# Kernel optimization log

Measured on AMD Instinct MI355X. Metric: run time of the kernel, lower is better.

Reference implementation:

```python
import jax, jax.numpy as jnp
import numpy as np

N = 50000      # nodes
E = 800000     # edges (avg degree 16)
IN, HID, OUT = 256, 128, 64
K, ALPHA = 4, 0.0  # APPNPConv(k=4, alpha=0.0)


def setup_inputs() -> dict:
    key = jax.random.key(0)
    ks = jax.random.split(key, 5)
    features = jax.random.normal(ks[0], (N, IN), jnp.float32)
    src = jax.random.randint(ks[1], (E,), 0, N, jnp.int32)
    dst = jax.random.randint(ks[2], (E,), 0, N, jnp.int32)
    W1 = jax.random.normal(ks[3], (IN, HID), jnp.float32) / np.float32(np.sqrt(IN))
    b1 = jnp.zeros((HID,), jnp.float32)
    W3 = jax.random.normal(ks[4], (HID, OUT), jnp.float32) / np.float32(np.sqrt(HID))
    b3 = jnp.zeros((OUT,), jnp.float32)
    return dict(features=features, src=src, dst=dst, W1=W1, b1=b1, W3=W3, b3=b3)


def _sym_norms(src, dst, n):
    # D_out^{-1/2} for source side, D_in^{-1/2} for destination side (DGL norm='both')
    ones = jnp.ones((src.shape[0],), jnp.float32)
    deg_out = jax.ops.segment_sum(ones, src, num_segments=n)
    deg_in = jax.ops.segment_sum(ones, dst, num_segments=n)
    return jnp.clip(deg_out, 1.0) ** -0.5, jnp.clip(deg_in, 1.0) ** -0.5


def _prop(x, src, dst, norm_src, norm_dst):
    # x: [N, D]. Symmetric-normalized SpMM: D_in^{-1/2} A D_out^{-1/2} x
    msg = (x * norm_src[:, None])[src]                       # [E, D] gather
    agg = jax.ops.segment_sum(msg, dst, num_segments=x.shape[0])  # [N, D] scatter-add
    return agg * norm_dst[:, None]


def reference(features, src, dst, W1, b1, W3, b3):
    ns, nd = _sym_norms(src, dst, N)
    # GraphConv 1 (weight-first since in_dim > hidden_dim; math identical either way)
    h = _prop(features @ W1, src, dst, ns, nd) + b1
    # dropout is identity in eval mode (training=False)
    # APPNPConv: k=4 power-iteration steps with teleport alpha=0.0
    h0 = h
    for _ in range(K):
        h = (1.0 - ALPHA) * _prop(h, src, dst, ns, nd) + ALPHA * h0
    # GraphConv 3
    out = _prop(h @ W3, src, dst, ns, nd) + b3
    return out
```

## Files before the change

### kernel.cpp

```cpp
#include <hip/hip_runtime.h>
#include <math.h>

#define N_NODES 50000
#define N_EDGES 800000
#define DIN 256
#define DHID 128
#define DOUT 64
#define CSTRIDE 64
#define ZROW N_NODES
#define HBLOCKS 256
#define HCHUNK (N_EDGES / HBLOCKS)
#define HWORDS (N_NODES / 4)
#define SLICE ((size_t)(N_NODES + 1) * 16)
#define NGROUPS (N_NODES / 4)
#define P2BLOCKS 196

#define SB_SENT 3125
#define SB_HS (SB_SENT + HBLOCKS)
#define SB_HD (SB_HS + HBLOCKS)
#define SB_TOT (SB_HD + 66)

__global__ void k_setup(const int* __restrict__ src, const int* __restrict__ dst,
                        unsigned int* __restrict__ pS, unsigned int* __restrict__ pD,
                        unsigned int* __restrict__ csr32,
                        const float* __restrict__ W1, const float* __restrict__ b1,
                        const float* __restrict__ W3,
                        float* __restrict__ W13, float* __restrict__ bb,
                        float* __restrict__ Y0, float* __restrict__ Y1) {
    __shared__ unsigned int h[HWORDS];
    int bx = blockIdx.x, t = threadIdx.x;
    if (bx < SB_SENT) {
        unsigned int v = (unsigned int)ZROW | ((unsigned int)ZROW << 16);
        uint2 o; o.x = v; o.y = v;
        ((uint2*)csr32)[bx * 256 + t] = o;
        return;
    }
    if (bx < SB_HD) {
        const int* idx = (bx < SB_HS) ? src : dst;
        unsigned int* outp = (bx < SB_HS) ? pS : pD;
        int hb = bx - ((bx < SB_HS) ? SB_SENT : SB_HS);
        for (int w = t; w < HWORDS; w += 256) h[w] = 0u;
        __syncthreads();
        int base = hb * HCHUNK;
        for (int i = t; i < HCHUNK; i += 256) {
            int s = idx[base + i];
            atomicAdd(&h[s >> 2], 1u << ((s & 3) << 3));
        }
        __syncthreads();
        outp += (size_t)hb * HWORDS;
        for (int w = t; w < HWORDS; w += 256) outp[w] = h[w];
        return;
    }
    int vb = bx - SB_HD;
    if (vb == 65) {
        if (t < 64) {
            int qq = t >> 4, c2 = t & 15;
            Y0[(size_t)qq * SLICE + ((size_t)ZROW << 4) + c2] = 0.f;
            Y1[(size_t)qq * SLICE + ((size_t)ZROW << 4) + c2] = 0.f;
        }
        return;
    }
    if (vb == 64) {
        if (t < DOUT) {
            float s = 0.f;
            for (int k = 0; k < DHID; ++k) s += b1[k] * W3[k * DOUT + t];
            bb[t] = s;
        }
        return;
    }
    int idx2 = vb * 256 + t;
    int i = idx2 >> 6, j = idx2 & 63;
    float s = 0.f;
    for (int k = 0; k < DHID; ++k) s += W1[i * DHID + k] * W3[k * DOUT + j];
    W13[idx2] = s;
}

__global__ void k_hpre(const unsigned int* __restrict__ pS,
                       const unsigned int* __restrict__ pD,
                       unsigned int* __restrict__ prefix,
                       int* __restrict__ deg_in,
                       float* __restrict__ ns, float* __restrict__ nd,
                       float* __restrict__ cc, int* __restrict__ dparts) {
    __shared__ unsigned int sdw[64][4];
    __shared__ unsigned int sow[64][4];
    __shared__ int lh[65];
    int t = threadIdx.x;
    if (t < 65) lh[t] = 0;
    int col = t >> 2, sub = t & 3;
    int wid = blockIdx.x * 64 + col;
    bool act = wid < HWORDS;
    unsigned int ps = 0, pd = 0;
    if (act) {
        int b0 = sub << 6;
#pragma unroll 4
        for (int b = b0; b < b0 + 64; ++b) {
            ps += pS[(size_t)b * HWORDS + wid];
            pd += pD[(size_t)b * HWORDS + wid];
        }
    }
    sdw[col][sub] = pd;
    sow[col][sub] = ps;
    __syncthreads();
    if (act) {
        unsigned int base = 0;
        for (int k = 0; k < sub; ++k) base += sdw[col][k];
        int b0 = sub << 6;
        unsigned int run = base;
        for (int b = b0; b < b0 + 64; ++b) {
            unsigned int w = pD[(size_t)b * HWORDS + wid];
            prefix[(size_t)b * HWORDS + wid] = run;
            run += w;
        }
        if (sub == 0) {
            unsigned int totd = sdw[col][0] + sdw[col][1] + sdw[col][2] + sdw[col][3];
            unsigned int toto = sow[col][0] + sow[col][1] + sow[col][2] + sow[col][3];
            unsigned int di[4] = {totd & 0xffu, (totd >> 8) & 0xffu,
                                  (totd >> 16) & 0xffu, totd >> 24};
            unsigned int dov[4] = {toto & 0xffu, (toto >> 8) & 0xffu,
                                   (toto >> 16) & 0xffu, toto >> 24};
            int4 dd; dd.x = (int)di[0]; dd.y = (int)di[1]; dd.z = (int)di[2]; dd.w = (int)di[3];
            *(int4*)(deg_in + (wid << 2)) = dd;
            float4 vns, vnd, vcc;
            float* pns = &vns.x; float* pnd = &vnd.x; float* pcc = &vcc.x;
#pragma unroll
            for (int q = 0; q < 4; ++q) {
                int bin = (int)di[q]; if (bin > 64) bin = 64;
                atomicAdd(&lh[bin], 1);
                unsigned int a = dov[q] < 1u ? 1u : dov[q];
                unsigned int b = di[q] < 1u ? 1u : di[q];
                float fa = 1.0f / sqrtf((float)a);
                float fb = 1.0f / sqrtf((float)b);
                pns[q] = fa; pnd[q] = fb; pcc[q] = fa * fb;
            }
            *(float4*)(ns + (wid << 2)) = vns;
            *(float4*)(nd + (wid << 2)) = vnd;
            *(float4*)(cc + (wid << 2)) = vcc;
        }
    }
    __syncthreads();
    if (t < 65) dparts[blockIdx.x * 65 + t] = lh[t];
}

__global__ void k_dscan(const int* __restrict__ dparts, int* __restrict__ offs) {
    __shared__ int colsum[65], binbase[65];
    int t = threadIdx.x;
    if (t < 65) {
        int s = 0;
        for (int b = 0; b < P2BLOCKS; ++b) s += dparts[b * 65 + t];
        colsum[t] = s;
    }
    __syncthreads();
    if (t == 0) {
        int run = 0;
        for (int k = 64; k >= 0; --k) { binbase[k] = run; run += colsum[k]; }
    }
    __syncthreads();
    if (t < 65) {
        int run = binbase[t];
        for (int b = 0; b < P2BLOCKS; ++b) { offs[b * 65 + t] = run; run += dparts[b * 65 + t]; }
    }
}

__global__ void k_dscatter(const int* __restrict__ deg_in, const int* __restrict__ offs,
                           const float* __restrict__ cc, const float* __restrict__ ns,
                           const float* __restrict__ nd,
                           int* __restrict__ perm, int* __restrict__ inv,
                           int* __restrict__ degP, float* __restrict__ ccP,
                           float* __restrict__ nsP, float* __restrict__ ndP) {
    __shared__ int off[65];
    int t = threadIdx.x;
    if (t < 65) off[t] = offs[blockIdx.x * 65 + t];
    __syncthreads();
    int wid = blockIdx.x * 64 + t;
    if (t < 64 && wid < HWORDS) {
        int4 d4 = *(const int4*)(deg_in + (wid << 2));
        int dd[4] = {d4.x, d4.y, d4.z, d4.w};
#pragma unroll
        for (int k = 0; k < 4; ++k) {
            int node = (wid << 2) + k;
            int bin = dd[k] > 64 ? 64 : dd[k];
            int slot = atomicAdd(&off[bin], 1);
            perm[slot] = node; inv[node] = slot;
            degP[slot] = dd[k];
            ccP[slot] = cc[node]; nsP[slot] = ns[node]; ndP[slot] = nd[node];
        }
    }
}

__global__ void k_fill(const int* __restrict__ src, const int* __restrict__ dst,
                       const unsigned int* __restrict__ prefix,
                       const int* __restrict__ inv,
                       unsigned short* __restrict__ csr) {
    __shared__ unsigned int h[HWORDS];
    int t = threadIdx.x;
    const unsigned int* prow = prefix + (size_t)blockIdx.x * HWORDS;
    for (int w = t; w < HWORDS; w += 256) h[w] = prow[w];
    __syncthreads();
    int base = blockIdx.x * HCHUNK;
    for (int i = t; i < HCHUNK; i += 256) {
        int s = src[base + i], d = dst[base + i];
        int sh = (d & 3) << 3;
        unsigned int old = atomicAdd(&h[d >> 2], 1u << sh);
        int slot = (int)((old >> sh) & 0xffu);
        csr[((size_t)inv[d] << 6) + slot] = (unsigned short)inv[s];
    }
}

__global__ void k_gemm(const float* __restrict__ X, const float* __restrict__ W13,
                       const float* __restrict__ ns, const int* __restrict__ inv,
                       float* __restrict__ Y) {
    __shared__ float As[16][68];
    __shared__ float Bs[16][64];
    int tid = threadIdx.x;
    int tx = tid & 15, ty = tid >> 4;
    int row0 = blockIdx.x * 64;
    float acc[4][4];
#pragma unroll
    for (int i = 0; i < 4; ++i)
#pragma unroll
        for (int j = 0; j < 4; ++j) acc[i][j] = 0.f;

    int lr = tid >> 2;
    int lk = (tid & 3) << 2;
    int arow = row0 + lr;
    if (arow > N_NODES - 1) arow = N_NODES - 1;

    for (int k0 = 0; k0 < DIN; k0 += 16) {
        float4 a = *(const float4*)(X + (size_t)arow * DIN + k0 + lk);
        As[lk + 0][lr] = a.x; As[lk + 1][lr] = a.y;
        As[lk + 2][lr] = a.z; As[lk + 3][lr] = a.w;
        float4 b = *(const float4*)(W13 + (size_t)(k0 + (tid >> 4)) * DOUT + ((tid & 15) << 2));
        *(float4*)&Bs[tid >> 4][(tid & 15) << 2] = b;
        __syncthreads();
#pragma unroll
        for (int k = 0; k < 16; ++k) {
            float4 av = *(const float4*)&As[k][ty << 2];
            float4 bv = *(const float4*)&Bs[k][tx << 2];
            float ar[4] = {av.x, av.y, av.z, av.w};
            float br[4] = {bv.x, bv.y, bv.z, bv.w};
#pragma unroll
            for (int i = 0; i < 4; ++i)
#pragma unroll
                for (int j = 0; j < 4; ++j) acc[i][j] += ar[i] * br[j];
        }
        __syncthreads();
    }
    int qq = tx >> 2;
    int co = (tx & 3) << 2;
#pragma unroll
    for (int i = 0; i < 4; ++i) {
        int row = row0 + (ty << 2) + i;
        if (row < N_NODES) {
            float nsr = ns[row];
            int prow = inv[row];
            float4 o;
            o.x = acc[i][0] * nsr; o.y = acc[i][1] * nsr;
            o.z = acc[i][2] * nsr; o.w = acc[i][3] * nsr;
            *(float4*)(Y + (size_t)qq * SLICE + ((size_t)prow << 4) + co) = o;
        }
    }
}


template <int MODE>
__launch_bounds__(256, 8)
__global__ void k_spmm(const float* __restrict__ xs, float* __restrict__ ys,
                       const unsigned short* __restrict__ csr,
                       const int* __restrict__ degP,
                       const float* __restrict__ ccP, const float* __restrict__ nsP,
                       const float* __restrict__ ndP,
                       const float* __restrict__ bb, const float* __restrict__ b3,
                       const int* __restrict__ perm) {
    __shared__ unsigned short rows[4][256];
    int wid  = threadIdx.x >> 6;
    int lane = threadIdx.x & 63;
    int q    = (blockIdx.x & 7) >> 1;
    int half = blockIdx.x & 1;
    int g    = (blockIdx.x >> 3) * 8 + wid * 2 + half;
    if (g >= NGROUPS) return;
    int node0 = g << 2;

    int nn = lane >> 4, sl = lane & 15;
    const uint2* crow = (const uint2*)(csr + ((size_t)(node0 + nn) << 6)) + sl;
    uint2 rv = *crow;
    unsigned short* bp = &rows[wid][(sl << 4) + nn];
    bp[0]  = (unsigned short)(rv.x & 0xffffu);
    bp[4]  = (unsigned short)(rv.x >> 16);
    bp[8]  = (unsigned short)(rv.y & 0xffffu);
    bp[12] = (unsigned short)(rv.y >> 16);

    int n0u = __builtin_amdgcn_readfirstlane(node0);
    int m = (degP[n0u] + 7) & ~7;

    int n = lane >> 4, e = (lane >> 2) & 3, c4 = lane & 3;
    const unsigned short* rd = &rows[wid][(e << 2) + n];
    const float* xq = xs + (size_t)q * SLICE + (c4 << 2);

    float ax = 0.f, ay = 0.f, az = 0.f, aw = 0.f;
#define LDV(T) const float4 v##T = *(const float4*)(xq + ((size_t)rd[16 * (T)] << 4))
#define ACCV(T) ax += v##T.x; ay += v##T.y; az += v##T.z; aw += v##T.w
    if (m <= 8) {
        LDV(0); LDV(1);
        ACCV(0); ACCV(1);
    } else if (m <= 16) {
        LDV(0); LDV(1); LDV(2); LDV(3);
        ACCV(0); ACCV(1); ACCV(2); ACCV(3);
    } else if (m <= 24) {
        LDV(0); LDV(1); LDV(2); LDV(3); LDV(4); LDV(5);
        ACCV(0); ACCV(1); ACCV(2); ACCV(3); ACCV(4); ACCV(5);
    } else if (m <= 32) {
        LDV(0); LDV(1); LDV(2); LDV(3); LDV(4); LDV(5); LDV(6); LDV(7);
        ACCV(0); ACCV(1); ACCV(2); ACCV(3); ACCV(4); ACCV(5); ACCV(6); ACCV(7);
    } else {
        for (int j2 = 0; j2 < m; j2 += 8) {
            int o = j2 << 2;
            const float4 a = *(const float4*)(xq + ((size_t)rd[o] << 4));
            const float4 b = *(const float4*)(xq + ((size_t)rd[o + 16] << 4));
            ax += a.x; ay += a.y; az += a.z; aw += a.w;
            ax += b.x; ay += b.y; az += b.z; aw += b.w;
        }
    }
#undef LDV
#undef ACCV
    ax += __shfl_xor(ax, 4);  ay += __shfl_xor(ay, 4);
    az += __shfl_xor(az, 4);  aw += __shfl_xor(aw, 4);
    ax += __shfl_xor(ax, 8);  ay += __shfl_xor(ay, 8);
    az += __shfl_xor(az, 8);  aw += __shfl_xor(aw, 8);

    int nodeL = node0 + n;
    int colq  = (q << 4) + (c4 << 2);
    float4 r;
    if (MODE == 0) {
        float cv = ccP[nodeL], nv = nsP[nodeL];
        float4 bv = *(const float4*)(bb + colq);
        r.x = cv * ax + nv * bv.x; r.y = cv * ay + nv * bv.y;
        r.z = cv * az + nv * bv.z; r.w = cv * aw + nv * bv.w;
    } else if (MODE == 1) {
        float cv = ccP[nodeL];
        r.x = cv * ax; r.y = cv * ay; r.z = cv * az; r.w = cv * aw;
    } else {
        float dv = ndP[nodeL];
        float4 bv = *(const float4*)(b3 + colq);
        r.x = dv * ax + bv.x; r.y = dv * ay + bv.y;
        r.z = dv * az + bv.z; r.w = dv * aw + bv.w;
    }
    if (e == 0) {
        if (MODE == 2) {
            int orow = perm[nodeL];
            *(float4*)(ys + ((size_t)orow << 6) + colq) = r;
        } else {
            *(float4*)(ys + (size_t)q * SLICE + ((size_t)nodeL << 4) + (c4 << 2)) = r;
        }
    }
}


extern "C" void kernel_launch(void* const* d_in, const int* in_sizes, int n_in,
                              void* d_out, int out_size, void* d_ws, size_t ws_size,
                              hipStream_t stream) {
    const float* X   = (const float*)d_in[0];
    const int*   src = (const int*)d_in[1];
    const int*   dst = (const int*)d_in[2];
    const float* W1  = (const float*)d_in[3];
    const float* b1  = (const float*)d_in[4];
    const float* W3  = (const float*)d_in[5];
    const float* b3  = (const float*)d_in[6];
    float* out = (float*)d_out;

    char* ws = (char*)d_ws;
    size_t off = 0;
    auto alloc = [&](size_t bytes) -> void* {
        void* p = ws + off;
        off = (off + bytes + 255) & ~(size_t)255;
        return p;
    };
    unsigned int*   pS     = (unsigned int*)alloc((size_t)HBLOCKS * HWORDS * 4);
    unsigned int*   pD     = (unsigned int*)alloc((size_t)HBLOCKS * HWORDS * 4);
    unsigned int*   pref   = (unsigned int*)alloc((size_t)HBLOCKS * HWORDS * 4);
    float*          Y0     = (float*)alloc(SLICE * 4 * 4);
    float*          Y1     = (float*)alloc(SLICE * 4 * 4);
    unsigned short* csr    = (unsigned short*)alloc((size_t)N_NODES * CSTRIDE * 2);
    int*            deg_in = (int*)alloc((size_t)N_NODES * 4);
    float*          ns     = (float*)alloc((size_t)N_NODES * 4);
    float*          nd     = (float*)alloc((size_t)N_NODES * 4);
    float*          cc     = (float*)alloc((size_t)N_NODES * 4);
    int*            perm   = (int*)alloc((size_t)N_NODES * 4);
    int*            inv    = (int*)alloc((size_t)N_NODES * 4);
    int*            degP   = (int*)alloc((size_t)N_NODES * 4);
    float*          ccP    = (float*)alloc((size_t)N_NODES * 4);
    float*          nsP    = (float*)alloc((size_t)N_NODES * 4);
    float*          ndP    = (float*)alloc((size_t)N_NODES * 4);
    int*            dparts = (int*)alloc((size_t)P2BLOCKS * 65 * 4);
    int*            offs   = (int*)alloc((size_t)P2BLOCKS * 65 * 4);
    float*          W13    = (float*)alloc((size_t)DIN * DOUT * 4);
    float*          bb     = (float*)alloc(DOUT * 4);

    const int sblk = 1563 * 8;

    k_setup<<<SB_TOT, 256, 0, stream>>>(src, dst, pS, pD, (unsigned int*)csr,
                                        W1, b1, W3, W13, bb, Y0, Y1);
    k_hpre<<<P2BLOCKS, 256, 0, stream>>>(pS, pD, pref, deg_in, ns, nd, cc, dparts);
    k_dscan<<<1, 128, 0, stream>>>(dparts, offs);
    k_dscatter<<<P2BLOCKS, 128, 0, stream>>>(deg_in, offs, cc, ns, nd,
                                             perm, inv, degP, ccP, nsP, ndP);
    k_fill<<<HBLOCKS, 256, 0, stream>>>(src, dst, pref, inv, csr);

    k_gemm<<<(N_NODES + 63) / 64, 256, 0, stream>>>(X, W13, ns, inv, Y0);

    k_spmm<0><<<sblk, 256, 0, stream>>>(Y0, Y1, csr, degP, ccP, nsP, ndP, bb, b3, perm);
    k_spmm<1><<<sblk, 256, 0, stream>>>(Y1, Y0, csr, degP, ccP, nsP, ndP, bb, b3, perm);
    k_spmm<1><<<sblk, 256, 0, stream>>>(Y0, Y1, csr, degP, ccP, nsP, ndP, bb, b3, perm);
    k_spmm<1><<<sblk, 256, 0, stream>>>(Y1, Y0, csr, degP, ccP, nsP, ndP, bb, b3, perm);
    k_spmm<1><<<sblk, 256, 0, stream>>>(Y0, Y1, csr, degP, ccP, nsP, ndP, bb, b3, perm);
    k_spmm<2><<<sblk, 256, 0, stream>>>(Y1, out, csr, degP, ccP, nsP, ndP, bb, b3, perm);
}
```

Measured before the change: 304.3 us.

## Process two node groups per wavefront in SpMM, fold degree scan into scatter

Each SpMM wavefront now handles two groups of four degree-sorted nodes (eight nodes), loading both CSR row tiles and interleaving their gathers so more memory loads are in flight per wave. The grid size is halved to match. The separate single-block degree-scan kernel is removed, and each scatter block recomputes the column totals and its own prefix from the partial histograms, which saves a launch but repeats that work in every block. The histogram block count is halved, which changes the prefix-sum loop bounds. The risks are extra register pressure, and a load imbalance from sizing the unrolled path by the first node's degree when the second group can have a different degree.

```diff
diff --git a/kernel.cpp b/kernel.cpp
--- a/kernel.cpp
+++ b/kernel.cpp
@@ -8,11 +8,12 @@
 #define DOUT 64
 #define CSTRIDE 64
 #define ZROW N_NODES
-#define HBLOCKS 256
+#define HBLOCKS 128
 #define HCHUNK (N_EDGES / HBLOCKS)
 #define HWORDS (N_NODES / 4)
 #define SLICE ((size_t)(N_NODES + 1) * 16)
 #define NGROUPS (N_NODES / 4)
+#define NPAIRS (NGROUPS / 2)
 #define P2BLOCKS 196
 
 #define SB_SENT 3125
@@ -91,9 +92,9 @@
     bool act = wid < HWORDS;
     unsigned int ps = 0, pd = 0;
     if (act) {
-        int b0 = sub << 6;
+        int b0 = sub << 5;
 #pragma unroll 4
-        for (int b = b0; b < b0 + 64; ++b) {
+        for (int b = b0; b < b0 + 32; ++b) {
             ps += pS[(size_t)b * HWORDS + wid];
             pd += pD[(size_t)b * HWORDS + wid];
         }
@@ -104,9 +105,9 @@
     if (act) {
         unsigned int base = 0;
         for (int k = 0; k < sub; ++k) base += sdw[col][k];
-        int b0 = sub << 6;
+        int b0 = sub << 5;
         unsigned int run = base;
-        for (int b = b0; b < b0 + 64; ++b) {
+        for (int b = b0; b < b0 + 32; ++b) {
             unsigned int w = pD[(size_t)b * HWORDS + wid];
             prefix[(size_t)b * HWORDS + wid] = run;
             run += w;
@@ -141,35 +142,31 @@
     if (t < 65) dparts[blockIdx.x * 65 + t] = lh[t];
 }
 
-__global__ void k_dscan(const int* __restrict__ dparts, int* __restrict__ offs) {
-    __shared__ int colsum[65], binbase[65];
-    int t = threadIdx.x;
-    if (t < 65) {
-        int s = 0;
-        for (int b = 0; b < P2BLOCKS; ++b) s += dparts[b * 65 + t];
-        colsum[t] = s;
-    }
-    __syncthreads();
-    if (t == 0) {
-        int run = 0;
-        for (int k = 64; k >= 0; --k) { binbase[k] = run; run += colsum[k]; }
-    }
-    __syncthreads();
-    if (t < 65) {
-        int run = binbase[t];
-        for (int b = 0; b < P2BLOCKS; ++b) { offs[b * 65 + t] = run; run += dparts[b * 65 + t]; }
-    }
-}
-
-__global__ void k_dscatter(const int* __restrict__ deg_in, const int* __restrict__ offs,
+__global__ void k_dscatter(const int* __restrict__ deg_in, const int* __restrict__ dparts,
                            const float* __restrict__ cc, const float* __restrict__ ns,
                            const float* __restrict__ nd,
                            int* __restrict__ perm, int* __restrict__ inv,
                            int* __restrict__ degP, float* __restrict__ ccP,
                            float* __restrict__ nsP, float* __restrict__ ndP) {
-    __shared__ int off[65];
+    __shared__ int colsum[65], pre[65], off[65];
     int t = threadIdx.x;
-    if (t < 65) off[t] = offs[blockIdx.x * 65 + t];
+    if (t < 65) {
+        int tot = 0, pr = 0;
+        int mybx = (int)blockIdx.x;
+        for (int b = 0; b < P2BLOCKS; ++b) {
+            int v = dparts[b * 65 + t];
+            tot += v;
+            if (b < mybx) pr += v;
+        }
+        colsum[t] = tot; pre[t] = pr;
+    }
+    __syncthreads();
+    if (t == 0) {
+        int run = 0;
+        for (int k = 64; k >= 0; --k) { int c = colsum[k]; colsum[k] = run; run += c; }
+    }
+    __syncthreads();
+    if (t < 65) off[t] = colsum[t] + pre[t];
     __syncthreads();
     int wid = blockIdx.x * 64 + t;
     if (t < 64 && wid < HWORDS) {
@@ -271,85 +268,124 @@
                        const float* __restrict__ ndP,
                        const float* __restrict__ bb, const float* __restrict__ b3,
                        const int* __restrict__ perm) {
-    __shared__ unsigned short rows[4][256];
+    __shared__ unsigned short rows[4][512];
     int wid  = threadIdx.x >> 6;
     int lane = threadIdx.x & 63;
     int q    = (blockIdx.x & 7) >> 1;
     int half = blockIdx.x & 1;
-    int g    = (blockIdx.x >> 3) * 8 + wid * 2 + half;
-    if (g >= NGROUPS) return;
-    int node0 = g << 2;
+    int p    = (blockIdx.x >> 3) * 8 + wid * 2 + half;
+    if (p >= NPAIRS) return;
+    int node0 = p << 3;
 
     int nn = lane >> 4, sl = lane & 15;
-    const uint2* crow = (const uint2*)(csr + ((size_t)(node0 + nn) << 6)) + sl;
-    uint2 rv = *crow;
-    unsigned short* bp = &rows[wid][(sl << 4) + nn];
-    bp[0]  = (unsigned short)(rv.x & 0xffffu);
-    bp[4]  = (unsigned short)(rv.x >> 16);
-    bp[8]  = (unsigned short)(rv.y & 0xffffu);
-    bp[12] = (unsigned short)(rv.y >> 16);
+    const uint2* crowA = (const uint2*)(csr + ((size_t)(node0 + nn) << 6)) + sl;
+    const uint2* crowB = (const uint2*)(csr + ((size_t)(node0 + 4 + nn) << 6)) + sl;
+    uint2 rva = *crowA;
+    uint2 rvb = *crowB;
+    unsigned short* bpA = &rows[wid][(sl << 4) + nn];
+    unsigned short* bpB = bpA + 256;
+    bpA[0]  = (unsigned short)(rva.x & 0xffffu);
+    bpA[4]  = (unsigned short)(rva.x >> 16);
+    bpA[8]  = (unsigned short)(rva.y & 0xffffu);
+    bpA[12] = (unsigned short)(rva.y >> 16);
+    bpB[0]  = (unsigned short)(rvb.x & 0xffffu);
+    bpB[4]  = (unsigned short)(rvb.x >> 16);
+    bpB[8]  = (unsigned short)(rvb.y & 0xffffu);
+    bpB[12] = (unsigned short)(rvb.y >> 16);
 
     int n0u = __builtin_amdgcn_readfirstlane(node0);
     int m = (degP[n0u] + 7) & ~7;
 
     int n = lane >> 4, e = (lane >> 2) & 3, c4 = lane & 3;
-    const unsigned short* rd = &rows[wid][(e << 2) + n];
+    const unsigned short* rdA = &rows[wid][(e << 2) + n];
+    const unsigned short* rdB = rdA + 256;
     const float* xq = xs + (size_t)q * SLICE + (c4 << 2);
 
-    float ax = 0.f, ay = 0.f, az = 0.f, aw = 0.f;
-#define LDV(T) const float4 v##T = *(const float4*)(xq + ((size_t)rd[16 * (T)] << 4))
-#define ACCV(T) ax += v##T.x; ay += v##T.y; az += v##T.z; aw += v##T.w
+    float aAx = 0.f, aAy = 0.f, aAz = 0.f, aAw = 0.f;
+    float aBx = 0.f, aBy = 0.f, aBz = 0.f, aBw = 0.f;
+#define LDA(T) const float4 vA##T = *(const float4*)(xq + ((size_t)rdA[16 * (T)] << 4))
+#define LDB(T) const float4 vB##T = *(const float4*)(xq + ((size_t)rdB[16 * (T)] << 4))
+#define ACA(T) aAx += vA##T.x; aAy += vA##T.y; aAz += vA##T.z; aAw += vA##T.w
+#define ACB(T) aBx += vB##T.x; aBy += vB##T.y; aBz += vB##T.z; aBw += vB##T.w
     if (m <= 8) {
-        LDV(0); LDV(1);
-        ACCV(0); ACCV(1);
+        LDA(0); LDA(1); LDB(0); LDB(1);
+        ACA(0); ACA(1); ACB(0); ACB(1);
     } else if (m <= 16) {
-        LDV(0); LDV(1); LDV(2); LDV(3);
-        ACCV(0); ACCV(1); ACCV(2); ACCV(3);
+        LDA(0); LDA(1); LDA(2); LDA(3); LDB(0); LDB(1); LDB(2); LDB(3);
+        ACA(0); ACA(1); ACA(2); ACA(3); ACB(0); ACB(1); ACB(2); ACB(3);
     } else if (m <= 24) {
-        LDV(0); LDV(1); LDV(2); LDV(3); LDV(4); LDV(5);
-        ACCV(0); ACCV(1); ACCV(2); ACCV(3); ACCV(4); ACCV(5);
+        LDA(0); LDA(1); LDA(2); LDA(3); LDA(4); LDA(5);
+        LDB(0); LDB(1);
+        ACA(0); ACA(1); ACA(2); ACA(3);
+        LDB(2); LDB(3); LDB(4); LDB(5);
+        ACA(4); ACA(5);
+        ACB(0); ACB(1); ACB(2); ACB(3); ACB(4); ACB(5);
     } else if (m <= 32) {
-        LDV(0); LDV(1); LDV(2); LDV(3); LDV(4); LDV(5); LDV(6); LDV(7);
-        ACCV(0); ACCV(1); ACCV(2); ACCV(3); ACCV(4); ACCV(5); ACCV(6); ACCV(7);
+        LDA(0); LDA(1); LDA(2); LDA(3); LDB(0); LDB(1); LDB(2); LDB(3);
+        ACA(0); ACA(1); ACA(2); ACA(3); ACB(0); ACB(1); ACB(2); ACB(3);
+        LDA(4); LDA(5); LDA(6); LDA(7); LDB(4); LDB(5); LDB(6); LDB(7);
+        ACA(4); ACA(5); ACA(6); ACA(7); ACB(4); ACB(5); ACB(6); ACB(7);
     } else {
         for (int j2 = 0; j2 < m; j2 += 8) {
             int o = j2 << 2;
-            const float4 a = *(const float4*)(xq + ((size_t)rd[o] << 4));
-            const float4 b = *(const float4*)(xq + ((size_t)rd[o + 16] << 4));
-            ax += a.x; ay += a.y; az += a.z; aw += a.w;
-            ax += b.x; ay += b.y; az += b.z; aw += b.w;
-        }
-    }
-#undef LDV
-#undef ACCV
-    ax += __shfl_xor(ax, 4);  ay += __shfl_xor(ay, 4);
-    az += __shfl_xor(az, 4);  aw += __shfl_xor(aw, 4);
-    ax += __shfl_xor(ax, 8);  ay += __shfl_xor(ay, 8);
-    az += __shfl_xor(az, 8);  aw += __shfl_xor(aw, 8);
-
-    int nodeL = node0 + n;
+            const float4 a0 = *(const float4*)(xq + ((size_t)rdA[o] << 4));
+            const float4 a1 = *(const float4*)(xq + ((size_t)rdA[o + 16] << 4));
+            const float4 b0 = *(const float4*)(xq + ((size_t)rdB[o] << 4));
+            const float4 b1 = *(const float4*)(xq + ((size_t)rdB[o + 16] << 4));
+            aAx += a0.x; aAy += a0.y; aAz += a0.z; aAw += a0.w;
+            aAx += a1.x; aAy += a1.y; aAz += a1.z; aAw += a1.w;
+            aBx += b0.x; aBy += b0.y; aBz += b0.z; aBw += b0.w;
+            aBx += b1.x; aBy += b1.y; aBz += b1.z; aBw += b1.w;
+        }
+    }
+#undef LDA
+#undef LDB
+#undef ACA
+#undef ACB
+    aAx += __shfl_xor(aAx, 4);  aAy += __shfl_xor(aAy, 4);
+    aAz += __shfl_xor(aAz, 4);  aAw += __shfl_xor(aAw, 4);
+    aBx += __shfl_xor(aBx, 4);  aBy += __shfl_xor(aBy, 4);
+    aBz += __shfl_xor(aBz, 4);  aBw += __shfl_xor(aBw, 4);
+    aAx += __shfl_xor(aAx, 8);  aAy += __shfl_xor(aAy, 8);
+    aAz += __shfl_xor(aAz, 8);  aAw += __shfl_xor(aAw, 8);
+    aBx += __shfl_xor(aBx, 8);  aBy += __shfl_xor(aBy, 8);
+    aBz += __shfl_xor(aBz, 8);  aBw += __shfl_xor(aBw, 8);
+
+    int nodeA = node0 + n;
+    int nodeB = node0 + 4 + n;
     int colq  = (q << 4) + (c4 << 2);
-    float4 r;
+    float4 rA, rB;
     if (MODE == 0) {
-        float cv = ccP[nodeL], nv = nsP[nodeL];
         float4 bv = *(const float4*)(bb + colq);
-        r.x = cv * ax + nv * bv.x; r.y = cv * ay + nv * bv.y;
-        r.z = cv * az + nv * bv.z; r.w = cv * aw + nv * bv.w;
+        float cvA = ccP[nodeA], nvA = nsP[nodeA];
+        rA.x = cvA * aAx + nvA * bv.x; rA.y = cvA * aAy + nvA * bv.y;
+        rA.z = cvA * aAz + nvA * bv.z; rA.w = cvA * aAw + nvA * bv.w;
+        float cvB = ccP[nodeB], nvB = nsP[nodeB];
+        rB.x = cvB * aBx + nvB * bv.x; rB.y = cvB * aBy + nvB * bv.y;
+        rB.z = cvB * aBz + nvB * bv.z; rB.w = cvB * aBw + nvB * bv.w;
     } else if (MODE == 1) {
-        float cv = ccP[nodeL];
-        r.x = cv * ax; r.y = cv * ay; r.z = cv * az; r.w = cv * aw;
+        float cvA = ccP[nodeA];
+        rA.x = cvA * aAx; rA.y = cvA * aAy; rA.z = cvA * aAz; rA.w = cvA * aAw;
+        float cvB = ccP[nodeB];
+        rB.x = cvB * aBx; rB.y = cvB * aBy; rB.z = cvB * aBz; rB.w = cvB * aBw;
     } else {
-        float dv = ndP[nodeL];
         float4 bv = *(const float4*)(b3 + colq);
-        r.x = dv * ax + bv.x; r.y = dv * ay + bv.y;
-        r.z = dv * az + bv.z; r.w = dv * aw + bv.w;
+        float dvA = ndP[nodeA];
+        rA.x = dvA * aAx + bv.x; rA.y = dvA * aAy + bv.y;
+        rA.z = dvA * aAz + bv.z; rA.w = dvA * aAw + bv.w;
+        float dvB = ndP[nodeB];
+        rB.x = dvB * aBx + bv.x; rB.y = dvB * aBy + bv.y;
+        rB.z = dvB * aBz + bv.z; rB.w = dvB * aBw + bv.w;
     }
     if (e == 0) {
         if (MODE == 2) {
-            int orow = perm[nodeL];
-            *(float4*)(ys + ((size_t)orow << 6) + colq) = r;
+            int orowA = perm[nodeA];
+            int orowB = perm[nodeB];
+            *(float4*)(ys + ((size_t)orowA << 6) + colq) = rA;
+            *(float4*)(ys + ((size_t)orowB << 6) + colq) = rB;
         } else {
-            *(float4*)(ys + (size_t)q * SLICE + ((size_t)nodeL << 4) + (c4 << 2)) = r;
+            *(float4*)(ys + (size_t)q * SLICE + ((size_t)nodeA << 4) + (c4 << 2)) = rA;
+            *(float4*)(ys + (size_t)q * SLICE + ((size_t)nodeB << 4) + (c4 << 2)) = rB;
         }
     }
 }
@@ -391,17 +427,15 @@
     float*          nsP    = (float*)alloc((size_t)N_NODES * 4);
     float*          ndP    = (float*)alloc((size_t)N_NODES * 4);
     int*            dparts = (int*)alloc((size_t)P2BLOCKS * 65 * 4);
-    int*            offs   = (int*)alloc((size_t)P2BLOCKS * 65 * 4);
     float*          W13    = (float*)alloc((size_t)DIN * DOUT * 4);
     float*          bb     = (float*)alloc(DOUT * 4);
 
-    const int sblk = 1563 * 8;
+    const int sblk = 782 * 8;
 
     k_setup<<<SB_TOT, 256, 0, stream>>>(src, dst, pS, pD, (unsigned int*)csr,
                                         W1, b1, W3, W13, bb, Y0, Y1);
     k_hpre<<<P2BLOCKS, 256, 0, stream>>>(pS, pD, pref, deg_in, ns, nd, cc, dparts);
-    k_dscan<<<1, 128, 0, stream>>>(dparts, offs);
-    k_dscatter<<<P2BLOCKS, 128, 0, stream>>>(deg_in, offs, cc, ns, nd,
+    k_dscatter<<<P2BLOCKS, 128, 0, stream>>>(deg_in, dparts, cc, ns, nd,
                                              perm, inv, degP, ccP, nsP, ndP);
     k_fill<<<HBLOCKS, 256, 0, stream>>>(src, dst, pref, inv, csr);
 
```

Result: no change. 309.4 us (+1.7%).

## Drop degree-sorted node permutation, use per-group max degree, fuse fill with GEMM

Applied to the files above, without the earlier changes.

Removes the degree-bucket sort (histogram, scan, scatter kernels) and the perm/inv indirection, so nodes stay in natural order. Each group of four nodes now stores its max in-degree rounded up to eight, which sets the SpMM loop trip count. The CSR fill and the X·W13 GEMM are merged into one launch, and the histogram block count is halved. This cuts setup kernels and launches but gives up degree-balanced grouping, so SpMM waves may see more divergence across mixed-degree nodes.

```diff
diff --git a/kernel.cpp b/kernel.cpp
--- a/kernel.cpp
+++ b/kernel.cpp
@@ -8,7 +8,7 @@
 #define DOUT 64
 #define CSTRIDE 64
 #define ZROW N_NODES
-#define HBLOCKS 256
+#define HBLOCKS 128
 #define HCHUNK (N_EDGES / HBLOCKS)
 #define HWORDS (N_NODES / 4)
 #define SLICE ((size_t)(N_NODES + 1) * 16)
@@ -56,6 +56,9 @@
         if (t < 64) {
             int qq = t >> 4, c2 = t & 15;
             Y0[(size_t)qq * SLICE + ((size_t)ZROW << 4) + c2] = 0.f;
+        } else if (t < 128) {
+            int t2 = t - 64;
+            int qq = t2 >> 4, c2 = t2 & 15;
             Y1[(size_t)qq * SLICE + ((size_t)ZROW << 4) + c2] = 0.f;
         }
         return;
@@ -78,22 +81,19 @@
 __global__ void k_hpre(const unsigned int* __restrict__ pS,
                        const unsigned int* __restrict__ pD,
                        unsigned int* __restrict__ prefix,
-                       int* __restrict__ deg_in,
                        float* __restrict__ ns, float* __restrict__ nd,
-                       float* __restrict__ cc, int* __restrict__ dparts) {
+                       float* __restrict__ cc, int* __restrict__ mG) {
     __shared__ unsigned int sdw[64][4];
     __shared__ unsigned int sow[64][4];
-    __shared__ int lh[65];
     int t = threadIdx.x;
-    if (t < 65) lh[t] = 0;
     int col = t >> 2, sub = t & 3;
     int wid = blockIdx.x * 64 + col;
     bool act = wid < HWORDS;
     unsigned int ps = 0, pd = 0;
     if (act) {
-        int b0 = sub << 6;
+        int b0 = sub << 5;
 #pragma unroll 4
-        for (int b = b0; b < b0 + 64; ++b) {
+        for (int b = b0; b < b0 + 32; ++b) {
             ps += pS[(size_t)b * HWORDS + wid];
             pd += pD[(size_t)b * HWORDS + wid];
         }
@@ -104,9 +104,9 @@
     if (act) {
         unsigned int base = 0;
         for (int k = 0; k < sub; ++k) base += sdw[col][k];
-        int b0 = sub << 6;
+        int b0 = sub << 5;
         unsigned int run = base;
-        for (int b = b0; b < b0 + 64; ++b) {
+        for (int b = b0; b < b0 + 32; ++b) {
             unsigned int w = pD[(size_t)b * HWORDS + wid];
             prefix[(size_t)b * HWORDS + wid] = run;
             run += w;
@@ -118,14 +118,12 @@
                                   (totd >> 16) & 0xffu, totd >> 24};
             unsigned int dov[4] = {toto & 0xffu, (toto >> 8) & 0xffu,
                                    (toto >> 16) & 0xffu, toto >> 24};
-            int4 dd; dd.x = (int)di[0]; dd.y = (int)di[1]; dd.z = (int)di[2]; dd.w = (int)di[3];
-            *(int4*)(deg_in + (wid << 2)) = dd;
             float4 vns, vnd, vcc;
             float* pns = &vns.x; float* pnd = &vnd.x; float* pcc = &vcc.x;
+            unsigned int mx = 0;
 #pragma unroll
             for (int q = 0; q < 4; ++q) {
-                int bin = (int)di[q]; if (bin > 64) bin = 64;
-                atomicAdd(&lh[bin], 1);
+                if (di[q] > mx) mx = di[q];
                 unsigned int a = dov[q] < 1u ? 1u : dov[q];
                 unsigned int b = di[q] < 1u ? 1u : di[q];
                 float fa = 1.0f / sqrtf((float)a);
@@ -135,96 +133,51 @@
             *(float4*)(ns + (wid << 2)) = vns;
             *(float4*)(nd + (wid << 2)) = vnd;
             *(float4*)(cc + (wid << 2)) = vcc;
-        }
-    }
-    __syncthreads();
-    if (t < 65) dparts[blockIdx.x * 65 + t] = lh[t];
-}
-
-__global__ void k_dscan(const int* __restrict__ dparts, int* __restrict__ offs) {
-    __shared__ int colsum[65], binbase[65];
-    int t = threadIdx.x;
-    if (t < 65) {
-        int s = 0;
-        for (int b = 0; b < P2BLOCKS; ++b) s += dparts[b * 65 + t];
-        colsum[t] = s;
-    }
-    __syncthreads();
-    if (t == 0) {
-        int run = 0;
-        for (int k = 64; k >= 0; --k) { binbase[k] = run; run += colsum[k]; }
-    }
-    __syncthreads();
-    if (t < 65) {
-        int run = binbase[t];
-        for (int b = 0; b < P2BLOCKS; ++b) { offs[b * 65 + t] = run; run += dparts[b * 65 + t]; }
-    }
-}
-
-__global__ void k_dscatter(const int* __restrict__ deg_in, const int* __restrict__ offs,
-                           const float* __restrict__ cc, const float* __restrict__ ns,
-                           const float* __restrict__ nd,
-                           int* __restrict__ perm, int* __restrict__ inv,
-                           int* __restrict__ degP, float* __restrict__ ccP,
-                           float* __restrict__ nsP, float* __restrict__ ndP) {
-    __shared__ int off[65];
-    int t = threadIdx.x;
-    if (t < 65) off[t] = offs[blockIdx.x * 65 + t];
-    __syncthreads();
-    int wid = blockIdx.x * 64 + t;
-    if (t < 64 && wid < HWORDS) {
-        int4 d4 = *(const int4*)(deg_in + (wid << 2));
-        int dd[4] = {d4.x, d4.y, d4.z, d4.w};
-#pragma unroll
-        for (int k = 0; k < 4; ++k) {
-            int node = (wid << 2) + k;
-            int bin = dd[k] > 64 ? 64 : dd[k];
-            int slot = atomicAdd(&off[bin], 1);
-            perm[slot] = node; inv[node] = slot;
-            degP[slot] = dd[k];
-            ccP[slot] = cc[node]; nsP[slot] = ns[node]; ndP[slot] = nd[node];
-        }
-    }
-}
-
-__global__ void k_fill(const int* __restrict__ src, const int* __restrict__ dst,
-                       const unsigned int* __restrict__ prefix,
-                       const int* __restrict__ inv,
-                       unsigned short* __restrict__ csr) {
-    __shared__ unsigned int h[HWORDS];
-    int t = threadIdx.x;
-    const unsigned int* prow = prefix + (size_t)blockIdx.x * HWORDS;
-    for (int w = t; w < HWORDS; w += 256) h[w] = prow[w];
-    __syncthreads();
-    int base = blockIdx.x * HCHUNK;
-    for (int i = t; i < HCHUNK; i += 256) {
-        int s = src[base + i], d = dst[base + i];
-        int sh = (d & 3) << 3;
-        unsigned int old = atomicAdd(&h[d >> 2], 1u << sh);
-        int slot = (int)((old >> sh) & 0xffu);
-        csr[((size_t)inv[d] << 6) + slot] = (unsigned short)inv[s];
-    }
-}
-
-__global__ void k_gemm(const float* __restrict__ X, const float* __restrict__ W13,
-                       const float* __restrict__ ns, const int* __restrict__ inv,
-                       float* __restrict__ Y) {
+            int m = ((int)mx + 7) & ~7;
+            mG[wid] = m > 64 ? 64 : m;
+        }
+    }
+}
+
+#define MB_FILL 128
+#define MB_GEMM 782
+#define MB_TOT (MB_FILL + MB_GEMM)
+
+__global__ void k_mid(const int* __restrict__ src, const int* __restrict__ dst,
+                      const unsigned int* __restrict__ prefix,
+                      unsigned short* __restrict__ csr,
+                      const float* __restrict__ X, const float* __restrict__ W13,
+                      const float* __restrict__ ns, float* __restrict__ Y) {
+    int bx = blockIdx.x, tid = threadIdx.x;
+    if (bx < MB_FILL) {
+        __shared__ unsigned int h[HWORDS];
+        const unsigned int* prow = prefix + (size_t)bx * HWORDS;
+        for (int w = tid; w < HWORDS; w += 256) h[w] = prow[w];
+        __syncthreads();
+        int base = bx * HCHUNK;
+        for (int i = tid; i < HCHUNK; i += 256) {
+            int s = src[base + i], d = dst[base + i];
+            int sh = (d & 3) << 3;
+            unsigned int old = atomicAdd(&h[d >> 2], 1u << sh);
+            int slot = (int)((old >> sh) & 0xffu);
+            csr[((size_t)d << 6) + slot] = (unsigned short)s;
+        }
+        return;
+    }
     __shared__ float As[16][68];
     __shared__ float Bs[16][64];
-    int tid = threadIdx.x;
+    int gb = bx - MB_FILL;
     int tx = tid & 15, ty = tid >> 4;
-    int row0 = blockIdx.x * 64;
+    int row0 = gb * 64;
     float acc[4][4];
 #pragma unroll
     for (int i = 0; i < 4; ++i)
 #pragma unroll
         for (int j = 0; j < 4; ++j) acc[i][j] = 0.f;
-
     int lr = tid >> 2;
     int lk = (tid & 3) << 2;
     int arow = row0 + lr;
     if (arow > N_NODES - 1) arow = N_NODES - 1;
-
     for (int k0 = 0; k0 < DIN; k0 += 16) {
         float4 a = *(const float4*)(X + (size_t)arow * DIN + k0 + lk);
         As[lk + 0][lr] = a.x; As[lk + 1][lr] = a.y;
@@ -252,11 +205,10 @@
         int row = row0 + (ty << 2) + i;
         if (row < N_NODES) {
             float nsr = ns[row];
-            int prow = inv[row];
             float4 o;
             o.x = acc[i][0] * nsr; o.y = acc[i][1] * nsr;
             o.z = acc[i][2] * nsr; o.w = acc[i][3] * nsr;
-            *(float4*)(Y + (size_t)qq * SLICE + ((size_t)prow << 4) + co) = o;
+            *(float4*)(Y + (size_t)qq * SLICE + ((size_t)row << 4) + co) = o;
         }
     }
 }
@@ -266,11 +218,10 @@
 __launch_bounds__(256, 8)
 __global__ void k_spmm(const float* __restrict__ xs, float* __restrict__ ys,
                        const unsigned short* __restrict__ csr,
-                       const int* __restrict__ degP,
-                       const float* __restrict__ ccP, const float* __restrict__ nsP,
-                       const float* __restrict__ ndP,
-                       const float* __restrict__ bb, const float* __restrict__ b3,
-                       const int* __restrict__ perm) {
+                       const int* __restrict__ mG,
+                       const float* __restrict__ cc, const float* __restrict__ ns,
+                       const float* __restrict__ nd,
+                       const float* __restrict__ bb, const float* __restrict__ b3) {
     __shared__ unsigned short rows[4][256];
     int wid  = threadIdx.x >> 6;
     int lane = threadIdx.x & 63;
@@ -289,8 +240,7 @@
     bp[8]  = (unsigned short)(rv.y & 0xffffu);
     bp[12] = (unsigned short)(rv.y >> 16);
 
-    int n0u = __builtin_amdgcn_readfirstlane(node0);
-    int m = (degP[n0u] + 7) & ~7;
+    int m = __builtin_amdgcn_readfirstlane(mG[g]);
 
     int n = lane >> 4, e = (lane >> 2) & 3, c4 = lane & 3;
     const unsigned short* rd = &rows[wid][(e << 2) + n];
@@ -331,23 +281,22 @@
     int colq  = (q << 4) + (c4 << 2);
     float4 r;
     if (MODE == 0) {
-        float cv = ccP[nodeL], nv = nsP[nodeL];
+        float cv = cc[nodeL], nv = ns[nodeL];
         float4 bv = *(const float4*)(bb + colq);
         r.x = cv * ax + nv * bv.x; r.y = cv * ay + nv * bv.y;
         r.z = cv * az + nv * bv.z; r.w = cv * aw + nv * bv.w;
     } else if (MODE == 1) {
-        float cv = ccP[nodeL];
+        float cv = cc[nodeL];
         r.x = cv * ax; r.y = cv * ay; r.z = cv * az; r.w = cv * aw;
     } else {
-        float dv = ndP[nodeL];
+        float dv = nd[nodeL];
         float4 bv = *(const float4*)(b3 + colq);
         r.x = dv * ax + bv.x; r.y = dv * ay + bv.y;
         r.z = dv * az + bv.z; r.w = dv * aw + bv.w;
     }
     if (e == 0) {
         if (MODE == 2) {
-            int orow = perm[nodeL];
-            *(float4*)(ys + ((size_t)orow << 6) + colq) = r;
+            *(float4*)(ys + ((size_t)nodeL << 6) + colq) = r;
         } else {
             *(float4*)(ys + (size_t)q * SLICE + ((size_t)nodeL << 4) + (c4 << 2)) = r;
         }
@@ -374,43 +323,30 @@
         off = (off + bytes + 255) & ~(size_t)255;
         return p;
     };
-    unsigned int*   pS     = (unsigned int*)alloc((size_t)HBLOCKS * HWORDS * 4);
-    unsigned int*   pD     = (unsigned int*)alloc((size_t)HBLOCKS * HWORDS * 4);
-    unsigned int*   pref   = (unsigned int*)alloc((size_t)HBLOCKS * HWORDS * 4);
-    float*          Y0     = (float*)alloc(SLICE * 4 * 4);
-    float*          Y1     = (float*)alloc(SLICE * 4 * 4);
-    unsigned short* csr    = (unsigned short*)alloc((size_t)N_NODES * CSTRIDE * 2);
-    int*            deg_in = (int*)alloc((size_t)N_NODES * 4);
-    float*          ns     = (float*)alloc((size_t)N_NODES * 4);
-    float*          nd     = (float*)alloc((size_t)N_NODES * 4);
-    float*          cc     = (float*)alloc((size_t)N_NODES * 4);
-    int*            perm   = (int*)alloc((size_t)N_NODES * 4);
-    int*            inv    = (int*)alloc((size_t)N_NODES * 4);
-    int*            degP   = (int*)alloc((size_t)N_NODES * 4);
-    float*          ccP    = (float*)alloc((size_t)N_NODES * 4);
-    float*          nsP    = (float*)alloc((size_t)N_NODES * 4);
-    float*          ndP    = (float*)alloc((size_t)N_NODES * 4);
-    int*            dparts = (int*)alloc((size_t)P2BLOCKS * 65 * 4);
-    int*            offs   = (int*)alloc((size_t)P2BLOCKS * 65 * 4);
-    float*          W13    = (float*)alloc((size_t)DIN * DOUT * 4);
-    float*          bb     = (float*)alloc(DOUT * 4);
+    unsigned int*   pS   = (unsigned int*)alloc((size_t)HBLOCKS * HWORDS * 4);
+    unsigned int*   pD   = (unsigned int*)alloc((size_t)HBLOCKS * HWORDS * 4);
+    unsigned int*   pref = (unsigned int*)alloc((size_t)HBLOCKS * HWORDS * 4);
+    float*          Y0   = (float*)alloc(SLICE * 4 * 4);
+    float*          Y1   = (float*)alloc(SLICE * 4 * 4);
+    unsigned short* csr  = (unsigned short*)alloc((size_t)N_NODES * CSTRIDE * 2);
+    float*          ns   = (float*)alloc((size_t)N_NODES * 4);
+    float*          nd   = (float*)alloc((size_t)N_NODES * 4);
+    float*          cc   = (float*)alloc((size_t)N_NODES * 4);
+    int*            mG   = (int*)alloc((size_t)NGROUPS * 4);
+    float*          W13  = (float*)alloc((size_t)DIN * DOUT * 4);
+    float*          bb   = (float*)alloc(DOUT * 4);
 
     const int sblk = 1563 * 8;
 
     k_setup<<<SB_TOT, 256, 0, stream>>>(src, dst, pS, pD, (unsigned int*)csr,
                                         W1, b1, W3, W13, bb, Y0, Y1);
-    k_hpre<<<P2BLOCKS, 256, 0, stream>>>(pS, pD, pref, deg_in, ns, nd, cc, dparts);
-    k_dscan<<<1, 128, 0, stream>>>(dparts, offs);
-    k_dscatter<<<P2BLOCKS, 128, 0, stream>>>(deg_in, offs, cc, ns, nd,
-                                             perm, inv, degP, ccP, nsP, ndP);
-    k_fill<<<HBLOCKS, 256, 0, stream>>>(src, dst, pref, inv, csr);
-
-    k_gemm<<<(N_NODES + 63) / 64, 256, 0, stream>>>(X, W13, ns, inv, Y0);
-
-    k_spmm<0><<<sblk, 256, 0, stream>>>(Y0, Y1, csr, degP, ccP, nsP, ndP, bb, b3, perm);
-    k_spmm<1><<<sblk, 256, 0, stream>>>(Y1, Y0, csr, degP, ccP, nsP, ndP, bb, b3, perm);
-    k_spmm<1><<<sblk, 256, 0, stream>>>(Y0, Y1, csr, degP, ccP, nsP, ndP, bb, b3, perm);
-    k_spmm<1><<<sblk, 256, 0, stream>>>(Y1, Y0, csr, degP, ccP, nsP, ndP, bb, b3, perm);
-    k_spmm<1><<<sblk, 256, 0, stream>>>(Y0, Y1, csr, degP, ccP, nsP, ndP, bb, b3, perm);
-    k_spmm<2><<<sblk, 256, 0, stream>>>(Y1, out, csr, degP, ccP, nsP, ndP, bb, b3, perm);
-}
+    k_hpre<<<P2BLOCKS, 256, 0, stream>>>(pS, pD, pref, ns, nd, cc, mG);
+    k_mid<<<MB_TOT, 256, 0, stream>>>(src, dst, pref, csr, X, W13, ns, Y0);
+
+    k_spmm<0><<<sblk, 256, 0, stream>>>(Y0, Y1, csr, mG, cc, ns, nd, bb, b3);
+    k_spmm<1><<<sblk, 256, 0, stream>>>(Y1, Y0, csr, mG, cc, ns, nd, bb, b3);
+    k_spmm<1><<<sblk, 256, 0, stream>>>(Y0, Y1, csr, mG, cc, ns, nd, bb, b3);
+    k_spmm<1><<<sblk, 256, 0, stream>>>(Y1, Y0, csr, mG, cc, ns, nd, bb, b3);
+    k_spmm<1><<<sblk, 256, 0, stream>>>(Y0, Y1, csr, mG, cc, ns, nd, bb, b3);
+    k_spmm<2><<<sblk, 256, 0, stream>>>(Y1, out, csr, mG, cc, ns, nd, bb, b3);
+}
```

Result: faster. 290.4 us (-4.5%).
